# Kernel optimization log

Hardware: AMD Instinct MI355X
Metric: run time of the kernel (lower is better)

Reference implementation:

```python
import jax, jax.numpy as jnp
import numpy as np

D = 128      # dims[0]: number of nodes
M1 = 256     # dims[1]
M2 = 128     # dims[2]
M3 = 1       # dims[3] (must be 1 for final squeeze)
B = 4096     # batch


def setup_inputs() -> dict:
    key = jax.random.key(0)
    ks = jax.random.split(key, 7)
    x = jax.random.normal(ks[0], (B, D), dtype=jnp.float32)
    # nn.Linear(D, D*M1): weight [D*M1, D], bias [D*M1]
    bnd1 = 1.0 / np.sqrt(D)
    W1 = jax.random.uniform(ks[1], (D * M1, D), minval=-bnd1, maxval=bnd1, dtype=jnp.float32)
    b1 = jax.random.uniform(ks[2], (D * M1,), minval=-bnd1, maxval=bnd1, dtype=jnp.float32)
    # An(D, M1, M2): weight [D, M1, M2], bias [D, M2]
    bnd_a = 1.0 / np.sqrt(M1)
    Wa = jax.random.uniform(ks[3], (D, M1, M2), minval=-bnd_a, maxval=bnd_a, dtype=jnp.float32)
    ba = jax.random.uniform(ks[4], (D, M2), minval=-bnd_a, maxval=bnd_a, dtype=jnp.float32)
    # An(D, M2, M3): weight [D, M2, M3], bias [D, M3]
    bnd_b = 1.0 / np.sqrt(M2)
    Wb = jax.random.uniform(ks[5], (D, M2, M3), minval=-bnd_b, maxval=bnd_b, dtype=jnp.float32)
    bb = jax.random.uniform(ks[6], (D, M3), minval=-bnd_b, maxval=bnd_b, dtype=jnp.float32)
    return {"x": x, "W1": W1, "b1": b1, "Wa": Wa, "ba": ba, "Wb": Wb, "bb": bb}


def reference(x, W1, b1, Wa, ba, Wb, bb):
    # a1: [B, D] -> [B, D*M1] -> [B, D, M1]
    h = (x @ W1.T + b1).reshape(B, D, M1)
    # An layer 1: sigmoid then per-node matmul + bias
    h = jnp.einsum('bni,nio->bno', jax.nn.sigmoid(h), Wa) + ba  # [B, D, M2]
    # An layer 2
    h = jnp.einsum('bni,nio->bno', jax.nn.sigmoid(h), Wb) + bb  # [B, D, 1]
    return h.squeeze(axis=2)  # [B, D]
```

## Files before the change

kernel.cpp:

```cpp
#include <hip/hip_runtime.h>

#define D_NODES 128
#define KD      128
#define M1_     256
#define M2_     128
#define B_      4096
#define BM      128
#define CI      64
#define NCH     4

typedef short bf16x8  __attribute__((ext_vector_type(8)));
typedef short short4v __attribute__((ext_vector_type(4)));
typedef float f32x4   __attribute__((ext_vector_type(4)));

#define MFMA16(a, b, c) __builtin_amdgcn_mfma_f32_16x16x32_bf16((a), (b), (c), 0, 0, 0)

__device__ __forceinline__ short f2b(float f) {
  unsigned u = __builtin_bit_cast(unsigned, f);
  u += 0x7FFFu + ((u >> 16) & 1u);
  return (short)(u >> 16);
}

__device__ __forceinline__ float sigmoidf_(float x) {
  float e = __builtin_amdgcn_exp2f(-1.44269504088896f * x);
  return __builtin_amdgcn_rcpf(1.0f + e);
}

__global__ void cvt_f2b_k(const float* __restrict__ in, short* __restrict__ out) {
  int i = (blockIdx.x * 256 + threadIdx.x) * 4;
  float4 f = *(const float4*)(in + i);
  short4v s; s[0] = f2b(f.x); s[1] = f2b(f.y); s[2] = f2b(f.z); s[3] = f2b(f.w);
  *(short4v*)(out + i) = s;
}

__global__ void trans_wa_k(const float* __restrict__ Wa, short* __restrict__ waT) {
  __shared__ float lt[64][129];
  int node = blockIdx.x >> 2, iblk = blockIdx.x & 3;
  int t = threadIdx.x;
  for (int j = 0; j < 32; ++j) {
    int e = j * 256 + t;
    int i = e >> 7, o = e & 127;
    lt[i][o] = Wa[(node * M1_ + iblk * 64 + i) * M2_ + o];
  }
  __syncthreads();
  int il = t & 63, ob = t >> 6;
  for (int j = 0; j < 32; ++j) {
    int o = j * 4 + ob;
    waT[(node * M2_ + o) * M1_ + iblk * 64 + il] = f2b(lt[il][o]);
  }
}

template <bool FAST>
__global__ __launch_bounds__(256, 2)
void fused_dag_k(const float* __restrict__ x,  const float* __restrict__ W1,
                 const float* __restrict__ b1, const float* __restrict__ Wa,
                 const float* __restrict__ ba, const float* __restrict__ Wb,
                 const float* __restrict__ bb, float* __restrict__ out,
                 const short* __restrict__ w1b, const short* __restrict__ waT,
                 const short* __restrict__ xb) {
  __shared__ __align__(16) short w1s[CI][136];
  __shared__ __align__(16) short wasT[M2_][72];
  __shared__ __align__(16) short h1s[BM][72];
  __shared__ float partial[BM][2];

  int gid = blockIdx.x;
  int xcd = gid & 7, ii = gid >> 3;
  int node = xcd * 16 + (ii >> 5);
  int tile = ii & 31;
  int b0 = tile * BM;

  int t = threadIdx.x;
  int w = t >> 6, l = t & 63;
  int n = l & 15, q = l >> 4;

  bf16x8 xa[2][4];
#pragma unroll
  for (int mt = 0; mt < 2; ++mt) {
#pragma unroll
    for (int kk = 0; kk < 4; ++kk) {
      int row = b0 + 32 * w + 16 * mt + n;
      int k0 = kk * 32 + q * 8;
      if (FAST) {
        xa[mt][kk] = *(const bf16x8*)(xb + row * KD + k0);
      } else {
        float4 f0 = *(const float4*)(x + row * KD + k0);
        float4 f1 = *(const float4*)(x + row * KD + k0 + 4);
        bf16x8 v;
        v[0] = f2b(f0.x); v[1] = f2b(f0.y); v[2] = f2b(f0.z); v[3] = f2b(f0.w);
        v[4] = f2b(f1.x); v[5] = f2b(f1.y); v[6] = f2b(f1.z); v[7] = f2b(f1.w);
        xa[mt][kk] = v;
      }
    }
  }

  f32x4 acc2[4][4];
#pragma unroll
  for (int a = 0; a < 4; ++a)
#pragma unroll
    for (int b = 0; b < 4; ++b) acc2[a][b] = (f32x4){0.f, 0.f, 0.f, 0.f};

  for (int c = 0; c < NCH; ++c) {
    __syncthreads();
    int R0 = node * M1_ + c * CI;
    if (FAST) {
#pragma unroll
      for (int j = 0; j < 4; ++j) {
        int ch = j * 256 + t;
        int r = ch >> 4, c8 = ch & 15;
        *(bf16x8*)(&w1s[r][c8 * 8]) = *(const bf16x8*)(w1b + (R0 + r) * KD + c8 * 8);
      }
#pragma unroll
      for (int j = 0; j < 4; ++j) {
        int ch = j * 256 + t;
        int r = ch >> 3, c8 = ch & 7;
        *(bf16x8*)(&wasT[r][c8 * 8]) =
            *(const bf16x8*)(waT + (node * M2_ + r) * M1_ + c * CI + c8 * 8);
      }
    } else {
#pragma unroll
      for (int j = 0; j < 8; ++j) {
        int g = j * 256 + t;
        int r = g >> 5, c4 = g & 31;
        float4 f = *(const float4*)(W1 + (R0 + r) * KD + c4 * 4);
        short4v s; s[0] = f2b(f.x); s[1] = f2b(f.y); s[2] = f2b(f.z); s[3] = f2b(f.w);
        *(short4v*)(&w1s[r][c4 * 4]) = s;
      }
      for (int j = 0; j < 32; ++j) {
        int e = j * 256 + t;
        int o = e & 127, i = e >> 7;
        wasT[o][i] = f2b(Wa[(node * M1_ + c * CI + i) * M2_ + o]);
      }
    }
    __syncthreads();

    f32x4 acc1[2][4];
#pragma unroll
    for (int a = 0; a < 2; ++a)
#pragma unroll
      for (int b = 0; b < 4; ++b) acc1[a][b] = (f32x4){0.f, 0.f, 0.f, 0.f};
#pragma unroll
    for (int kk = 0; kk < 4; ++kk) {
      bf16x8 wb[4];
#pragma unroll
      for (int it = 0; it < 4; ++it)
        wb[it] = *(const bf16x8*)(&w1s[16 * it + n][kk * 32 + q * 8]);
#pragma unroll
      for (int mt = 0; mt < 2; ++mt)
#pragma unroll
        for (int it = 0; it < 4; ++it)
          acc1[mt][it] = MFMA16(xa[mt][kk], wb[it], acc1[mt][it]);
    }
#pragma unroll
    for (int it = 0; it < 4; ++it) {
      float b1v = b1[node * M1_ + c * CI + 16 * it + n];
#pragma unroll
      for (int mt = 0; mt < 2; ++mt) {
        int rowb = 32 * w + 16 * mt + 4 * q;
#pragma unroll
        for (int r = 0; r < 4; ++r) {
          float s = sigmoidf_(acc1[mt][it][r] + b1v);
          h1s[rowb + r][16 * it + n] = f2b(s);
        }
      }
    }
    __syncthreads();

    int R2 = 64 * (w >> 1), O2 = 64 * (w & 1);
#pragma unroll
    for (int kk = 0; kk < 2; ++kk) {
      bf16x8 ha[4], wa[4];
#pragma unroll
      for (int mt = 0; mt < 4; ++mt)
        ha[mt] = *(const bf16x8*)(&h1s[R2 + 16 * mt + n][kk * 32 + q * 8]);
#pragma unroll
      for (int ot = 0; ot < 4; ++ot)
        wa[ot] = *(const bf16x8*)(&wasT[O2 + 16 * ot + n][kk * 32 + q * 8]);
#pragma unroll
      for (int mt = 0; mt < 4; ++mt)
#pragma unroll
        for (int ot = 0; ot < 4; ++ot)
          acc2[mt][ot] = MFMA16(ha[mt], wa[ot], acc2[mt][ot]);
    }
  }

  int R2 = 64 * (w >> 1), O2 = 64 * (w & 1);
#pragma unroll
  for (int mt = 0; mt < 4; ++mt) {
    f32x4 rowsum = (f32x4){0.f, 0.f, 0.f, 0.f};
#pragma unroll
    for (int ot = 0; ot < 4; ++ot) {
      int o = O2 + 16 * ot + n;
      float bav = ba[node * M2_ + o];
      float wbv = Wb[node * M2_ + o];
#pragma unroll
      for (int r = 0; r < 4; ++r)
        rowsum[r] += sigmoidf_(acc2[mt][ot][r] + bav) * wbv;
    }
#pragma unroll
    for (int r = 0; r < 4; ++r) {
      float v = rowsum[r];
      v += __shfl_xor(v, 1);
      v += __shfl_xor(v, 2);
      v += __shfl_xor(v, 4);
      v += __shfl_xor(v, 8);
      if (n == 0) partial[R2 + 16 * mt + 4 * q + r][w & 1] = v;
    }
  }
  __syncthreads();
  if (t < BM) {
    out[(size_t)(b0 + t) * D_NODES + node] = partial[t][0] + partial[t][1] + bb[node];
  }
}

extern "C" void kernel_launch(void* const* d_in, const int* in_sizes, int n_in,
                              void* d_out, int out_size, void* d_ws, size_t ws_size,
                              hipStream_t stream) {
  const float* x  = (const float*)d_in[0];
  const float* W1 = (const float*)d_in[1];
  const float* b1 = (const float*)d_in[2];
  const float* Wa = (const float*)d_in[3];
  const float* ba = (const float*)d_in[4];
  const float* Wb = (const float*)d_in[5];
  const float* bb = (const float*)d_in[6];
  float* out = (float*)d_out;

  const size_t W1_ELEMS = (size_t)D_NODES * M1_ * KD;
  const size_t WA_ELEMS = (size_t)D_NODES * M1_ * M2_;
  const size_t X_ELEMS  = (size_t)B_ * KD;
  const size_t NEED = (W1_ELEMS + WA_ELEMS + X_ELEMS) * sizeof(short);

  if (ws_size >= NEED) {
    short* w1b = (short*)d_ws;
    short* waT = w1b + W1_ELEMS;
    short* xb  = waT + WA_ELEMS;
    cvt_f2b_k<<<(int)(W1_ELEMS / 1024), 256, 0, stream>>>(W1, w1b);
    cvt_f2b_k<<<(int)(X_ELEMS / 1024), 256, 0, stream>>>(x, xb);
    trans_wa_k<<<D_NODES * 4, 256, 0, stream>>>(Wa, waT);
    fused_dag_k<true><<<4096, 256, 0, stream>>>(x, W1, b1, Wa, ba, Wb, bb, out, w1b, waT, xb);
  } else {
    fused_dag_k<false><<<4096, 256, 0, stream>>>(x, W1, b1, Wa, ba, Wb, bb, out,
                                                 nullptr, nullptr, nullptr);
  }
}
```

Measured before the change: 152.2 us.

## Use 512-thread blocks with 8 waves and swap MFMA operands for vectorized h1 stores

Doubles the block to 8 waves so each wave handles 16 rows in the first GEMM and a 32x64 tile in the second, halving per-wave accumulators and register pressure and allowing higher occupancy (launch bounds 512,4). The first GEMM now computes W1·x (operands swapped), so each lane holds 4 consecutive M1 outputs and can store sigmoid results to shared memory as a packed short4 and load the bias as a vector. Smaller per-wave tiles mean less register reuse of LDS fragments, and the block-wide syncs now span more waves.

New measurement: 142.7 us. 1.07x faster.

```diff
diff --git a/kernel.cpp b/kernel.cpp
--- a/kernel.cpp
+++ b/kernel.cpp
@@ -51,7 +51,7 @@
 }
 
 template <bool FAST>
-__global__ __launch_bounds__(256, 2)
+__global__ __launch_bounds__(512, 4)
 void fused_dag_k(const float* __restrict__ x,  const float* __restrict__ W1,
                  const float* __restrict__ b1, const float* __restrict__ Wa,
                  const float* __restrict__ ba, const float* __restrict__ Wb,
@@ -73,29 +73,28 @@
   int w = t >> 6, l = t & 63;
   int n = l & 15, q = l >> 4;
 
-  bf16x8 xa[2][4];
-#pragma unroll
-  for (int mt = 0; mt < 2; ++mt) {
+  bf16x8 xa[4];
+  {
+    int row = b0 + 16 * w + n;
 #pragma unroll
     for (int kk = 0; kk < 4; ++kk) {
-      int row = b0 + 32 * w + 16 * mt + n;
       int k0 = kk * 32 + q * 8;
       if (FAST) {
-        xa[mt][kk] = *(const bf16x8*)(xb + row * KD + k0);
+        xa[kk] = *(const bf16x8*)(xb + row * KD + k0);
       } else {
         float4 f0 = *(const float4*)(x + row * KD + k0);
         float4 f1 = *(const float4*)(x + row * KD + k0 + 4);
         bf16x8 v;
         v[0] = f2b(f0.x); v[1] = f2b(f0.y); v[2] = f2b(f0.z); v[3] = f2b(f0.w);
         v[4] = f2b(f1.x); v[5] = f2b(f1.y); v[6] = f2b(f1.z); v[7] = f2b(f1.w);
-        xa[mt][kk] = v;
-      }
-    }
-  }
-
-  f32x4 acc2[4][4];
-#pragma unroll
-  for (int a = 0; a < 4; ++a)
+        xa[kk] = v;
+      }
+    }
+  }
+
+  f32x4 acc2[2][4];
+#pragma unroll
+  for (int a = 0; a < 2; ++a)
 #pragma unroll
     for (int b = 0; b < 4; ++b) acc2[a][b] = (f32x4){0.f, 0.f, 0.f, 0.f};
 
@@ -104,88 +103,80 @@
     int R0 = node * M1_ + c * CI;
     if (FAST) {
 #pragma unroll
-      for (int j = 0; j < 4; ++j) {
-        int ch = j * 256 + t;
+      for (int j = 0; j < 2; ++j) {
+        int ch = j * 512 + t;
         int r = ch >> 4, c8 = ch & 15;
         *(bf16x8*)(&w1s[r][c8 * 8]) = *(const bf16x8*)(w1b + (R0 + r) * KD + c8 * 8);
       }
 #pragma unroll
-      for (int j = 0; j < 4; ++j) {
-        int ch = j * 256 + t;
+      for (int j = 0; j < 2; ++j) {
+        int ch = j * 512 + t;
         int r = ch >> 3, c8 = ch & 7;
         *(bf16x8*)(&wasT[r][c8 * 8]) =
             *(const bf16x8*)(waT + (node * M2_ + r) * M1_ + c * CI + c8 * 8);
       }
     } else {
 #pragma unroll
-      for (int j = 0; j < 8; ++j) {
-        int g = j * 256 + t;
+      for (int j = 0; j < 4; ++j) {
+        int g = j * 512 + t;
         int r = g >> 5, c4 = g & 31;
         float4 f = *(const float4*)(W1 + (R0 + r) * KD + c4 * 4);
         short4v s; s[0] = f2b(f.x); s[1] = f2b(f.y); s[2] = f2b(f.z); s[3] = f2b(f.w);
         *(short4v*)(&w1s[r][c4 * 4]) = s;
       }
-      for (int j = 0; j < 32; ++j) {
-        int e = j * 256 + t;
+      for (int j = 0; j < 16; ++j) {
+        int e = j * 512 + t;
         int o = e & 127, i = e >> 7;
         wasT[o][i] = f2b(Wa[(node * M1_ + c * CI + i) * M2_ + o]);
       }
     }
     __syncthreads();
 
-    f32x4 acc1[2][4];
-#pragma unroll
-    for (int a = 0; a < 2; ++a)
-#pragma unroll
-      for (int b = 0; b < 4; ++b) acc1[a][b] = (f32x4){0.f, 0.f, 0.f, 0.f};
+    f32x4 acc1[4];
+#pragma unroll
+    for (int a = 0; a < 4; ++a) acc1[a] = (f32x4){0.f, 0.f, 0.f, 0.f};
 #pragma unroll
     for (int kk = 0; kk < 4; ++kk) {
-      bf16x8 wb[4];
+      bf16x8 wf[4];
 #pragma unroll
       for (int it = 0; it < 4; ++it)
-        wb[it] = *(const bf16x8*)(&w1s[16 * it + n][kk * 32 + q * 8]);
+        wf[it] = *(const bf16x8*)(&w1s[16 * it + n][kk * 32 + q * 8]);
+#pragma unroll
+      for (int it = 0; it < 4; ++it)
+        acc1[it] = MFMA16(wf[it], xa[kk], acc1[it]);
+    }
+#pragma unroll
+    for (int it = 0; it < 4; ++it) {
+      f32x4 b1v = *(const f32x4*)(b1 + node * M1_ + c * CI + 16 * it + 4 * q);
+      short4v s;
+#pragma unroll
+      for (int r = 0; r < 4; ++r)
+        s[r] = f2b(sigmoidf_(acc1[it][r] + b1v[r]));
+      *(short4v*)(&h1s[16 * w + n][16 * it + 4 * q]) = s;
+    }
+    __syncthreads();
+
+    int R2 = 32 * (w & 3), O2 = 64 * (w >> 2);
+#pragma unroll
+    for (int kk = 0; kk < 2; ++kk) {
+      bf16x8 ha[2], wa[4];
 #pragma unroll
       for (int mt = 0; mt < 2; ++mt)
-#pragma unroll
-        for (int it = 0; it < 4; ++it)
-          acc1[mt][it] = MFMA16(xa[mt][kk], wb[it], acc1[mt][it]);
-    }
-#pragma unroll
-    for (int it = 0; it < 4; ++it) {
-      float b1v = b1[node * M1_ + c * CI + 16 * it + n];
-#pragma unroll
-      for (int mt = 0; mt < 2; ++mt) {
-        int rowb = 32 * w + 16 * mt + 4 * q;
-#pragma unroll
-        for (int r = 0; r < 4; ++r) {
-          float s = sigmoidf_(acc1[mt][it][r] + b1v);
-          h1s[rowb + r][16 * it + n] = f2b(s);
-        }
-      }
-    }
-    __syncthreads();
-
-    int R2 = 64 * (w >> 1), O2 = 64 * (w & 1);
-#pragma unroll
-    for (int kk = 0; kk < 2; ++kk) {
-      bf16x8 ha[4], wa[4];
-#pragma unroll
-      for (int mt = 0; mt < 4; ++mt)
         ha[mt] = *(const bf16x8*)(&h1s[R2 + 16 * mt + n][kk * 32 + q * 8]);
 #pragma unroll
       for (int ot = 0; ot < 4; ++ot)
         wa[ot] = *(const bf16x8*)(&wasT[O2 + 16 * ot + n][kk * 32 + q * 8]);
 #pragma unroll
-      for (int mt = 0; mt < 4; ++mt)
+      for (int mt = 0; mt < 2; ++mt)
 #pragma unroll
         for (int ot = 0; ot < 4; ++ot)
           acc2[mt][ot] = MFMA16(ha[mt], wa[ot], acc2[mt][ot]);
     }
   }
 
-  int R2 = 64 * (w >> 1), O2 = 64 * (w & 1);
-#pragma unroll
-  for (int mt = 0; mt < 4; ++mt) {
+  int R2 = 32 * (w & 3), O2 = 64 * (w >> 2);
+#pragma unroll
+  for (int mt = 0; mt < 2; ++mt) {
     f32x4 rowsum = (f32x4){0.f, 0.f, 0.f, 0.f};
 #pragma unroll
     for (int ot = 0; ot < 4; ++ot) {
@@ -203,7 +194,7 @@
       v += __shfl_xor(v, 2);
       v += __shfl_xor(v, 4);
       v += __shfl_xor(v, 8);
-      if (n == 0) partial[R2 + 16 * mt + 4 * q + r][w & 1] = v;
+      if (n == 0) partial[R2 + 16 * mt + 4 * q + r][w >> 2] = v;
     }
   }
   __syncthreads();
@@ -236,9 +227,9 @@
     cvt_f2b_k<<<(int)(W1_ELEMS / 1024), 256, 0, stream>>>(W1, w1b);
     cvt_f2b_k<<<(int)(X_ELEMS / 1024), 256, 0, stream>>>(x, xb);
     trans_wa_k<<<D_NODES * 4, 256, 0, stream>>>(Wa, waT);
-    fused_dag_k<true><<<4096, 256, 0, stream>>>(x, W1, b1, Wa, ba, Wb, bb, out, w1b, waT, xb);
+    fused_dag_k<true><<<4096, 512, 0, stream>>>(x, W1, b1, Wa, ba, Wb, bb, out, w1b, waT, xb);
   } else {
-    fused_dag_k<false><<<4096, 256, 0, stream>>>(x, W1, b1, Wa, ba, Wb, bb, out,
+    fused_dag_k<false><<<4096, 512, 0, stream>>>(x, W1, b1, Wa, ba, Wb, bb, out,
                                                  nullptr, nullptr, nullptr);
   }
 }
```

## Stage whole per-node weights in LDS once and keep h1 per-warp

Applied to the files above, without the earlier changes.

Each block now handles 256 batch rows with 512 threads and loads the full per-node W1 slice and transposed Wa into XOR-swizzled shared memory once, instead of reloading 64-row chunks each iteration. Every warp owns 32 rows and writes its sigmoid(h1) tile into a private shared buffer. That removes the block-wide barriers inside the chunk loop and the final cross-warp partial reduction, and outputs are written straight from the warps. The cost is about 130KB of shared memory per block, which may limit occupancy, plus more accumulator registers (acc2 of 2x8 tiles) with launch_bounds(512,2).

Result: faster. 128.5 us (-15.6%).

```diff
diff --git a/kernel.cpp b/kernel.cpp
--- a/kernel.cpp
+++ b/kernel.cpp
@@ -5,7 +5,8 @@
 #define M1_     256
 #define M2_     128
 #define B_      4096
-#define BM      128
+#define BM      256
+#define WROWS   32
 #define CI      64
 #define NCH     4
 
@@ -51,164 +52,183 @@
 }
 
 template <bool FAST>
-__global__ __launch_bounds__(256, 2)
+__global__ __launch_bounds__(512, 2)
 void fused_dag_k(const float* __restrict__ x,  const float* __restrict__ W1,
                  const float* __restrict__ b1, const float* __restrict__ Wa,
                  const float* __restrict__ ba, const float* __restrict__ Wb,
                  const float* __restrict__ bb, float* __restrict__ out,
                  const short* __restrict__ w1b, const short* __restrict__ waT,
                  const short* __restrict__ xb) {
-  __shared__ __align__(16) short w1s[CI][136];
-  __shared__ __align__(16) short wasT[M2_][72];
-  __shared__ __align__(16) short h1s[BM][72];
-  __shared__ float partial[BM][2];
+  __shared__ __align__(16) short w1s[M1_ * KD];
+  __shared__ __align__(16) short was[M2_ * M1_];
+  __shared__ __align__(16) short h1w[8 * 16 * CI];
 
   int gid = blockIdx.x;
   int xcd = gid & 7, ii = gid >> 3;
-  int node = xcd * 16 + (ii >> 5);
-  int tile = ii & 31;
+  int node = xcd * 16 + (ii >> 4);
+  int tile = ii & 15;
   int b0 = tile * BM;
 
   int t = threadIdx.x;
   int w = t >> 6, l = t & 63;
-  int n = l & 15, q = l >> 4;
+  int n15 = l & 15, q = l >> 4;
+
+  if (FAST) {
+    const short* w1n = w1b + (size_t)node * M1_ * KD;
+    const short* wan = waT + (size_t)node * M2_ * M1_;
+    bf16x8 t1[8], t2[8];
+#pragma unroll
+    for (int j = 0; j < 8; ++j) t1[j] = *(const bf16x8*)(w1n + (j * 512 + t) * 8);
+#pragma unroll
+    for (int j = 0; j < 8; ++j) t2[j] = *(const bf16x8*)(wan + (j * 512 + t) * 8);
+#pragma unroll
+    for (int j = 0; j < 8; ++j) {
+      int s = j * 512 + t;
+      int row = s >> 4, g = s & 15;
+      *(bf16x8*)(&w1s[row * KD + ((g ^ (row & 7)) << 3)]) = t1[j];
+    }
+#pragma unroll
+    for (int j = 0; j < 8; ++j) {
+      int s = j * 512 + t;
+      int row = s >> 5, g = s & 31;
+      *(bf16x8*)(&was[row * M1_ + ((g ^ (row & 7)) << 3)]) = t2[j];
+    }
+  } else {
+#pragma unroll
+    for (int j = 0; j < 8; ++j) {
+      int s = j * 512 + t;
+      int row = s >> 4, g = s & 15;
+      const float* src = W1 + ((size_t)node * M1_ + row) * KD + g * 8;
+      float4 f0 = *(const float4*)(src);
+      float4 f1 = *(const float4*)(src + 4);
+      bf16x8 v;
+      v[0] = f2b(f0.x); v[1] = f2b(f0.y); v[2] = f2b(f0.z); v[3] = f2b(f0.w);
+      v[4] = f2b(f1.x); v[5] = f2b(f1.y); v[6] = f2b(f1.z); v[7] = f2b(f1.w);
+      *(bf16x8*)(&w1s[row * KD + ((g ^ (row & 7)) << 3)]) = v;
+    }
+    for (int j = 0; j < 8; ++j) {
+      int s = j * 512 + t;
+      int o = s >> 5, g = s & 31;
+      bf16x8 v;
+#pragma unroll
+      for (int e = 0; e < 8; ++e)
+        v[e] = f2b(Wa[((size_t)node * M1_ + g * 8 + e) * M2_ + o]);
+      *(bf16x8*)(&was[o * M1_ + ((g ^ (o & 7)) << 3)]) = v;
+    }
+  }
 
   bf16x8 xa[2][4];
+  {
+    int rb = b0 + w * WROWS;
+#pragma unroll
+    for (int mt = 0; mt < 2; ++mt) {
+      int row = rb + mt * 16 + n15;
+#pragma unroll
+      for (int kk = 0; kk < 4; ++kk) {
+        int k0 = kk * 32 + q * 8;
+        if (FAST) {
+          xa[mt][kk] = *(const bf16x8*)(xb + row * KD + k0);
+        } else {
+          float4 f0 = *(const float4*)(x + row * KD + k0);
+          float4 f1 = *(const float4*)(x + row * KD + k0 + 4);
+          bf16x8 v;
+          v[0] = f2b(f0.x); v[1] = f2b(f0.y); v[2] = f2b(f0.z); v[3] = f2b(f0.w);
+          v[4] = f2b(f1.x); v[5] = f2b(f1.y); v[6] = f2b(f1.z); v[7] = f2b(f1.w);
+          xa[mt][kk] = v;
+        }
+      }
+    }
+  }
+
+  __syncthreads();
+
+  f32x4 acc2[2][8];
+#pragma unroll
+  for (int a = 0; a < 2; ++a)
+#pragma unroll
+    for (int b = 0; b < 8; ++b) acc2[a][b] = (f32x4){0.f, 0.f, 0.f, 0.f};
+
+  short* myh1 = &h1w[w * 16 * CI];
+  int swz = n15 & 7;
+
+  for (int c = 0; c < NCH; ++c) {
+    f32x4 acc1[4][2];
+#pragma unroll
+    for (int a = 0; a < 4; ++a)
+#pragma unroll
+      for (int b = 0; b < 2; ++b) acc1[a][b] = (f32x4){0.f, 0.f, 0.f, 0.f};
+#pragma unroll
+    for (int kk = 0; kk < 4; ++kk) {
+      int gsw = (4 * kk + q) ^ swz;
+#pragma unroll
+      for (int it = 0; it < 4; ++it) {
+        int row = c * CI + it * 16 + n15;
+        bf16x8 wf = *(const bf16x8*)(&w1s[row * KD + (gsw << 3)]);
+        acc1[it][0] = MFMA16(wf, xa[0][kk], acc1[it][0]);
+        acc1[it][1] = MFMA16(wf, xa[1][kk], acc1[it][1]);
+      }
+    }
+
+    bf16x8 wa[8][2];
+#pragma unroll
+    for (int ot = 0; ot < 8; ++ot) {
+      int o = ot * 16 + n15;
+#pragma unroll
+      for (int kk = 0; kk < 2; ++kk) {
+        int g = (c * 8 + kk * 4 + q) ^ swz;
+        wa[ot][kk] = *(const bf16x8*)(&was[o * M1_ + (g << 3)]);
+      }
+    }
+
+    const float* b1c = b1 + node * M1_ + c * CI;
+#pragma unroll
+    for (int mt = 0; mt < 2; ++mt) {
+#pragma unroll
+      for (int it = 0; it < 4; ++it) {
+        f32x4 bv = *(const f32x4*)(b1c + it * 16 + q * 4);
+        short4v s4;
+#pragma unroll
+        for (int r = 0; r < 4; ++r)
+          s4[r] = f2b(sigmoidf_(acc1[it][mt][r] + bv[r]));
+        int gi = (2 * it + (q >> 1)) ^ swz;
+        *(short4v*)(&myh1[n15 * CI + (gi << 3) + (q & 1) * 4]) = s4;
+      }
+#pragma unroll
+      for (int kk = 0; kk < 2; ++kk) {
+        int g = (4 * kk + q) ^ swz;
+        bf16x8 ha = *(const bf16x8*)(&myh1[n15 * CI + (g << 3)]);
+#pragma unroll
+        for (int ot = 0; ot < 8; ++ot)
+          acc2[mt][ot] = MFMA16(ha, wa[ot][kk], acc2[mt][ot]);
+      }
+    }
+  }
+
+  const float* ban = ba + node * M2_;
+  const float* wbn = Wb + node * M2_;
+  float bbv = bb[node];
 #pragma unroll
   for (int mt = 0; mt < 2; ++mt) {
-#pragma unroll
-    for (int kk = 0; kk < 4; ++kk) {
-      int row = b0 + 32 * w + 16 * mt + n;
-      int k0 = kk * 32 + q * 8;
-      if (FAST) {
-        xa[mt][kk] = *(const bf16x8*)(xb + row * KD + k0);
-      } else {
-        float4 f0 = *(const float4*)(x + row * KD + k0);
-        float4 f1 = *(const float4*)(x + row * KD + k0 + 4);
-        bf16x8 v;
-        v[0] = f2b(f0.x); v[1] = f2b(f0.y); v[2] = f2b(f0.z); v[3] = f2b(f0.w);
-        v[4] = f2b(f1.x); v[5] = f2b(f1.y); v[6] = f2b(f1.z); v[7] = f2b(f1.w);
-        xa[mt][kk] = v;
-      }
-    }
-  }
-
-  f32x4 acc2[4][4];
-#pragma unroll
-  for (int a = 0; a < 4; ++a)
-#pragma unroll
-    for (int b = 0; b < 4; ++b) acc2[a][b] = (f32x4){0.f, 0.f, 0.f, 0.f};
-
-  for (int c = 0; c < NCH; ++c) {
-    __syncthreads();
-    int R0 = node * M1_ + c * CI;
-    if (FAST) {
-#pragma unroll
-      for (int j = 0; j < 4; ++j) {
-        int ch = j * 256 + t;
-        int r = ch >> 4, c8 = ch & 15;
-        *(bf16x8*)(&w1s[r][c8 * 8]) = *(const bf16x8*)(w1b + (R0 + r) * KD + c8 * 8);
-      }
-#pragma unroll
-      for (int j = 0; j < 4; ++j) {
-        int ch = j * 256 + t;
-        int r = ch >> 3, c8 = ch & 7;
-        *(bf16x8*)(&wasT[r][c8 * 8]) =
-            *(const bf16x8*)(waT + (node * M2_ + r) * M1_ + c * CI + c8 * 8);
-      }
-    } else {
-#pragma unroll
-      for (int j = 0; j < 8; ++j) {
-        int g = j * 256 + t;
-        int r = g >> 5, c4 = g & 31;
-        float4 f = *(const float4*)(W1 + (R0 + r) * KD + c4 * 4);
-        short4v s; s[0] = f2b(f.x); s[1] = f2b(f.y); s[2] = f2b(f.z); s[3] = f2b(f.w);
-        *(short4v*)(&w1s[r][c4 * 4]) = s;
-      }
-      for (int j = 0; j < 32; ++j) {
-        int e = j * 256 + t;
-        int o = e & 127, i = e >> 7;
-        wasT[o][i] = f2b(Wa[(node * M1_ + c * CI + i) * M2_ + o]);
-      }
-    }
-    __syncthreads();
-
-    f32x4 acc1[2][4];
-#pragma unroll
-    for (int a = 0; a < 2; ++a)
-#pragma unroll
-      for (int b = 0; b < 4; ++b) acc1[a][b] = (f32x4){0.f, 0.f, 0.f, 0.f};
-#pragma unroll
-    for (int kk = 0; kk < 4; ++kk) {
-      bf16x8 wb[4];
-#pragma unroll
-      for (int it = 0; it < 4; ++it)
-        wb[it] = *(const bf16x8*)(&w1s[16 * it + n][kk * 32 + q * 8]);
-#pragma unroll
-      for (int mt = 0; mt < 2; ++mt)
-#pragma unroll
-        for (int it = 0; it < 4; ++it)
-          acc1[mt][it] = MFMA16(xa[mt][kk], wb[it], acc1[mt][it]);
-    }
-#pragma unroll
-    for (int it = 0; it < 4; ++it) {
-      float b1v = b1[node * M1_ + c * CI + 16 * it + n];
-#pragma unroll
-      for (int mt = 0; mt < 2; ++mt) {
-        int rowb = 32 * w + 16 * mt + 4 * q;
-#pragma unroll
-        for (int r = 0; r < 4; ++r) {
-          float s = sigmoidf_(acc1[mt][it][r] + b1v);
-          h1s[rowb + r][16 * it + n] = f2b(s);
-        }
-      }
-    }
-    __syncthreads();
-
-    int R2 = 64 * (w >> 1), O2 = 64 * (w & 1);
-#pragma unroll
-    for (int kk = 0; kk < 2; ++kk) {
-      bf16x8 ha[4], wa[4];
-#pragma unroll
-      for (int mt = 0; mt < 4; ++mt)
-        ha[mt] = *(const bf16x8*)(&h1s[R2 + 16 * mt + n][kk * 32 + q * 8]);
-#pragma unroll
-      for (int ot = 0; ot < 4; ++ot)
-        wa[ot] = *(const bf16x8*)(&wasT[O2 + 16 * ot + n][kk * 32 + q * 8]);
-#pragma unroll
-      for (int mt = 0; mt < 4; ++mt)
-#pragma unroll
-        for (int ot = 0; ot < 4; ++ot)
-          acc2[mt][ot] = MFMA16(ha[mt], wa[ot], acc2[mt][ot]);
-    }
-  }
-
-  int R2 = 64 * (w >> 1), O2 = 64 * (w & 1);
-#pragma unroll
-  for (int mt = 0; mt < 4; ++mt) {
-    f32x4 rowsum = (f32x4){0.f, 0.f, 0.f, 0.f};
-#pragma unroll
-    for (int ot = 0; ot < 4; ++ot) {
-      int o = O2 + 16 * ot + n;
-      float bav = ba[node * M2_ + o];
-      float wbv = Wb[node * M2_ + o];
+    f32x4 rs = (f32x4){0.f, 0.f, 0.f, 0.f};
+#pragma unroll
+    for (int ot = 0; ot < 8; ++ot) {
+      int o = ot * 16 + n15;
+      float bav = ban[o];
+      float wbv = wbn[o];
 #pragma unroll
       for (int r = 0; r < 4; ++r)
-        rowsum[r] += sigmoidf_(acc2[mt][ot][r] + bav) * wbv;
+        rs[r] += sigmoidf_(acc2[mt][ot][r] + bav) * wbv;
     }
 #pragma unroll
     for (int r = 0; r < 4; ++r) {
-      float v = rowsum[r];
+      float v = rs[r];
       v += __shfl_xor(v, 1);
       v += __shfl_xor(v, 2);
       v += __shfl_xor(v, 4);
       v += __shfl_xor(v, 8);
-      if (n == 0) partial[R2 + 16 * mt + 4 * q + r][w & 1] = v;
-    }
-  }
-  __syncthreads();
-  if (t < BM) {
-    out[(size_t)(b0 + t) * D_NODES + node] = partial[t][0] + partial[t][1] + bb[node];
+      if (n15 == 0)
+        out[(size_t)(b0 + w * WROWS + mt * 16 + q * 4 + r) * D_NODES + node] = v + bbv;
+    }
   }
 }
 
@@ -229,6 +249,8 @@
   const size_t X_ELEMS  = (size_t)B_ * KD;
   const size_t NEED = (W1_ELEMS + WA_ELEMS + X_ELEMS) * sizeof(short);
 
+  const int GRID = D_NODES * (B_ / BM);
+
   if (ws_size >= NEED) {
     short* w1b = (short*)d_ws;
     short* waT = w1b + W1_ELEMS;
@@ -236,9 +258,9 @@
     cvt_f2b_k<<<(int)(W1_ELEMS / 1024), 256, 0, stream>>>(W1, w1b);
     cvt_f2b_k<<<(int)(X_ELEMS / 1024), 256, 0, stream>>>(x, xb);
     trans_wa_k<<<D_NODES * 4, 256, 0, stream>>>(Wa, waT);
-    fused_dag_k<true><<<4096, 256, 0, stream>>>(x, W1, b1, Wa, ba, Wb, bb, out, w1b, waT, xb);
+    fused_dag_k<true><<<GRID, 512, 0, stream>>>(x, W1, b1, Wa, ba, Wb, bb, out, w1b, waT, xb);
   } else {
-    fused_dag_k<false><<<4096, 256, 0, stream>>>(x, W1, b1, Wa, ba, Wb, bb, out,
+    fused_dag_k<false><<<GRID, 512, 0, stream>>>(x, W1, b1, Wa, ba, Wb, bb, out,
                                                  nullptr, nullptr, nullptr);
   }
 }
```
